# Kernel optimization log

Hardware: AMD Instinct MI355X
Metric: run time of the kernel (lower is better)

The kernel has to match this reference:

```python
import jax, jax.numpy as jnp
import numpy as np

N = 100000   # nodes
E = 3200000  # edges (avg degree 32)
D = 512      # dim_latent
NEG_SLOPE = 0.01  # nn.LeakyReLU default


def setup_inputs() -> dict:
    key = jax.random.key(0)
    ks = jax.random.split(key, 14)
    weight = jax.random.normal(ks[0], (N,), dtype=jnp.float32)
    significance = jax.random.randint(ks[1], (N,), 0, 2, dtype=jnp.int32)
    src = jax.random.randint(ks[2], (E,), 0, N, dtype=jnp.int32)
    dst = jax.random.randint(ks[3], (E,), 0, N, dtype=jnp.int32)
    emb_table = jax.random.normal(ks[4], (2, 2), dtype=jnp.float32)
    lin_W = jax.random.normal(ks[5], (3, D), dtype=jnp.float32) / np.sqrt(3.0)
    lin_b = jnp.zeros((D,), dtype=jnp.float32)
    s = 1.0 / np.sqrt(D)
    W0 = jax.random.normal(ks[6], (D, D), dtype=jnp.float32) * s
    b0 = jnp.zeros((D,), dtype=jnp.float32)
    W1 = jax.random.normal(ks[7], (D, D), dtype=jnp.float32) * s
    b1 = jnp.zeros((D,), dtype=jnp.float32)
    W2 = jax.random.normal(ks[8], (D, D), dtype=jnp.float32) * s
    b2 = jnp.zeros((D,), dtype=jnp.float32)
    pred_W = jax.random.normal(ks[9], (D, 1), dtype=jnp.float32) * s
    pred_b = jnp.zeros((1,), dtype=jnp.float32)
    return {"weight": weight, "significance": significance, "src": src, "dst": dst,
            "emb_table": emb_table, "lin_W": lin_W, "lin_b": lin_b,
            "W0": W0, "b0": b0, "W1": W1, "b1": b1, "W2": W2, "b2": b2,
            "pred_W": pred_W, "pred_b": pred_b}


def _gcn_layer(feat, src, dst, n_out, n_in, W, b):
    # DGL GraphConv norm='both' with self-loops already folded into degrees.
    h = feat * n_out[:, None]                                   # [N, D] src-normalize
    agg = jax.ops.segment_sum(h[src], dst, num_segments=N)      # SpMM aggregate
    agg = agg + h                                               # self-loop message
    agg = agg * n_in[:, None]                                   # dst-normalize
    return agg @ W + b


def reference(weight, significance, src, dst, emb_table, lin_W, lin_b,
              W0, b0, W1, b1, W2, b2, pred_W, pred_b):
    ones = jnp.ones((E,), dtype=jnp.float32)
    deg_out = jax.ops.segment_sum(ones, src, num_segments=N) + 1.0  # +1 self-loop
    deg_in = jax.ops.segment_sum(ones, dst, num_segments=N) + 1.0
    n_out = jax.lax.rsqrt(deg_out)
    n_in = jax.lax.rsqrt(deg_in)

    sig = emb_table[significance]                            # [N, 2]
    feats = jnp.concatenate([weight[:, None], sig], axis=1)  # [N, 3]
    feats = feats @ lin_W + lin_b                            # [N, D]

    h = _gcn_layer(feats, src, dst, n_out, n_in, W0, b0)
    for W, b in ((W1, b1), (W2, b2)):
        h = jnp.where(h >= 0, h, NEG_SLOPE * h)              # LeakyReLU
        h = _gcn_layer(h, src, dst, n_out, n_in, W, b)

    # NOTE: original forward's `if self.train:` is always truthy (method object),
    # so it always returns the prediction logits.
    logits = h @ pred_W + pred_b                             # [N, 1]
    return logits
```

## Files before the change

kernel.cpp:

```cpp
#include <hip/hip_runtime.h>

#define N_NODES 100000
#define M_PAD 100096
#define N_EDGES 3200000
#define DIM 512
#define SLOTS 80
#define NEG_SLOPE 0.01f

typedef _Float16 f16;
typedef _Float16 f16x8 __attribute__((ext_vector_type(8)));
typedef float f32x4 __attribute__((ext_vector_type(4)));

__device__ __forceinline__ void load_lds16(const void* g, void* l) {
  __builtin_amdgcn_global_load_lds(
      (const __attribute__((address_space(1))) void*)g,
      (__attribute__((address_space(3))) void*)l, 16, 0, 0);
}


__global__ void k_pre(const int* __restrict__ src, const int* __restrict__ dst,
                      int* __restrict__ cnt_o, int* __restrict__ cnt_i,
                      int* __restrict__ ell) {
  int e = blockIdx.x * blockDim.x + threadIdx.x;
  if (e < N_EDGES) {
    int s = src[e];
    atomicAdd(&cnt_o[s], 1);
    int d = dst[e];
    int p = atomicAdd(&cnt_i[d], 1);
    if (p < SLOTS) ell[(size_t)d * SLOTS + p] = s;
  }
}

__global__ void k_norms(const int* __restrict__ cnt_o, const int* __restrict__ cnt_i,
                        float* __restrict__ n_out, float* __restrict__ n_in) {
  int i = blockIdx.x * blockDim.x + threadIdx.x;
  if (i < N_NODES) {
    n_out[i] = rsqrtf((float)cnt_o[i] + 1.0f);
    n_in[i] = rsqrtf((float)cnt_i[i] + 1.0f);
  }
}

__global__ void k_wt(const float* __restrict__ W0, const float* __restrict__ W1,
                     f16* __restrict__ Wt) {
  int idx = blockIdx.x * blockDim.x + threadIdx.x;
  int l = idx >> 18;
  int r = idx & 262143;
  int n = r >> 9, k = r & 511;
  const float* W = (l == 0) ? W0 : W1;
  Wt[idx] = (f16)W[k * DIM + n];
}

__global__ void k_wp(const float* __restrict__ W2, const float* __restrict__ b2,
                     const float* __restrict__ pW, const float* __restrict__ pb,
                     float* __restrict__ wt_vec, float* __restrict__ c_out) {
  int k = blockIdx.x, lane = threadIdx.x;
  if (k < DIM) {
    float s = 0.f;
    for (int n = lane; n < DIM; n += 64) s += W2[k * DIM + n] * pW[n];
#pragma unroll
    for (int off = 32; off; off >>= 1) s += __shfl_down(s, off, 64);
    if (lane == 0) wt_vec[k] = s;
  } else {
    float s = 0.f;
    for (int n = lane; n < DIM; n += 64) s += b2[n] * pW[n];
#pragma unroll
    for (int off = 32; off; off >>= 1) s += __shfl_down(s, off, 64);
    if (lane == 0) c_out[0] = s + pb[0];
  }
}


__global__ void k_feats(const float* __restrict__ weight, const int* __restrict__ sig,
                        const float* __restrict__ emb, const float* __restrict__ linW,
                        const float* __restrict__ linb, const float* __restrict__ n_out,
                        f16* __restrict__ Xs) {
  int wid = threadIdx.x >> 6, lane = threadIdx.x & 63;
  int node = blockIdx.x * 4 + wid;
  float w = weight[node];
  int sg = sig[node];
  float s0 = emb[sg * 2], s1 = emb[sg * 2 + 1];
  float no = n_out[node];
  int d0 = lane * 8;
  f16x8 v;
#pragma unroll
  for (int k = 0; k < 8; k++) {
    int d = d0 + k;
    float f = (w * linW[d] + s0 * linW[DIM + d] + s1 * linW[2 * DIM + d] + linb[d]) * no;
    v[k] = (f16)f;
  }
  *(f16x8*)(Xs + (size_t)node * DIM + d0) = v;
}

__global__ void k_spmm(const f16* __restrict__ Xs, f16* __restrict__ A,
                       const int* __restrict__ ell, const int* __restrict__ cnt_i,
                       const float* __restrict__ n_in) {
  int wid = threadIdx.x >> 6, lane = threadIdx.x & 63;
  int node = blockIdx.x * 4 + wid;
  int d0 = lane * 8;
  float acc[8];
  {
    f16x8 v = *(const f16x8*)(Xs + (size_t)node * DIM + d0);
#pragma unroll
    for (int k = 0; k < 8; k++) acc[k] = (float)v[k];
  }
  int deg = cnt_i[node];
  if (deg > SLOTS) deg = SLOTS;
  const int* erow = ell + (size_t)node * SLOTS;
  const f16* base = Xs + d0;
  int j = 0;
  for (; j + 8 <= deg; j += 8) {
    int ix[8];
#pragma unroll
    for (int u = 0; u < 8; u++) ix[u] = erow[j + u];
    f16x8 v[8];
#pragma unroll
    for (int u = 0; u < 8; u++) v[u] = *(const f16x8*)(base + (size_t)ix[u] * DIM);
#pragma unroll
    for (int u = 0; u < 8; u++)
#pragma unroll
      for (int k = 0; k < 8; k++) acc[k] += (float)v[u][k];
  }
  for (; j < deg; ++j) {
    int sn = erow[j];
    f16x8 v = *(const f16x8*)(base + (size_t)sn * DIM);
#pragma unroll
    for (int k = 0; k < 8; k++) acc[k] += (float)v[k];
  }
  float ni = n_in[node];
  f16x8 o;
#pragma unroll
  for (int k = 0; k < 8; k++) o[k] = (f16)(acc[k] * ni);
  __builtin_nontemporal_store(o, (f16x8*)(A + (size_t)node * DIM + d0));
}

__global__ __launch_bounds__(256) void k_gemm(const f16* __restrict__ A, const f16* __restrict__ Wt,
                                              const float* __restrict__ bias,
                                              const float* __restrict__ n_out,
                                              f16* __restrict__ Y,
                                              const float* __restrict__ wt_vec,
                                              float* __restrict__ yv) {
  __shared__ __align__(1024) char smem[32768];
  __shared__ float yred[128];
  const int tid = threadIdx.x;
  const int wid = tid >> 6, lane = tid & 63;
  const int lr = lane & 15, lk = lane >> 4;
  const int wr = wid >> 1, wc = wid & 1;
  const int cb = blockIdx.x * 128;
  const int rb = blockIdx.y * 128;
  const int ls = lane >> 3;
  const int ss = lane & 7;

  f32x4 acc[4][4];
#pragma unroll
  for (int i = 0; i < 4; i++)
#pragma unroll
    for (int j = 0; j < 4; j++) acc[i][j] = (f32x4){0.f, 0.f, 0.f, 0.f};

  for (int kb = 0; kb < DIM; kb += 64) {
#pragma unroll
    for (int i = 0; i < 4; i++) {
      int c = wid * 4 + i;
      int r = c * 8 + ls;
      int goff = (ss * 16) ^ ((r & 7) << 4);
      const char* ga = (const char*)A + ((size_t)(rb + r) * DIM + kb) * 2 + goff;
      load_lds16(ga, smem + c * 1024);
      const char* gw = (const char*)Wt + ((size_t)(cb + r) * DIM + kb) * 2 + goff;
      load_lds16(gw, smem + 16384 + c * 1024);
    }
    __syncthreads();
#pragma unroll
    for (int kk = 0; kk < 2; kk++) {
      f16x8 a[4], b[4];
#pragma unroll
      for (int fm = 0; fm < 4; fm++) {
        int row = wr * 64 + fm * 16 + lr;
        int byt = row * 128 + ((kk * 64 + lk * 16) ^ ((row & 7) << 4));
        a[fm] = *(const f16x8*)(smem + byt);
      }
#pragma unroll
      for (int fn = 0; fn < 4; fn++) {
        int row = wc * 64 + fn * 16 + lr;
        int byt = row * 128 + ((kk * 64 + lk * 16) ^ ((row & 7) << 4));
        b[fn] = *(const f16x8*)(smem + 16384 + byt);
      }
#pragma unroll
      for (int fm = 0; fm < 4; fm++)
#pragma unroll
        for (int fn = 0; fn < 4; fn++)
          acc[fm][fn] = __builtin_amdgcn_mfma_f32_16x16x32_f16(a[fm], b[fn], acc[fm][fn], 0, 0, 0);
    }
    __syncthreads();
  }

  if (yv == nullptr) {
#pragma unroll
    for (int fn = 0; fn < 4; fn++) {
      int col = cb + wc * 64 + fn * 16 + lr;
      float bv = bias[col];
#pragma unroll
      for (int fm = 0; fm < 4; fm++) {
#pragma unroll
        for (int r = 0; r < 4; r++) {
          int row = rb + wr * 64 + fm * 16 + lk * 4 + r;
          if (row < N_NODES) {
            float v = acc[fm][fn][r] + bv;
            v = (v >= 0.f) ? v : NEG_SLOPE * v;
            v *= n_out[row];
            Y[(size_t)row * DIM + col] = (f16)v;
          }
        }
      }
    }
  } else {
    if (tid < 128) yred[tid] = 0.f;
    __syncthreads();
#pragma unroll
    for (int fm = 0; fm < 4; fm++) {
#pragma unroll
      for (int r = 0; r < 4; r++) {
        int rloc = wr * 64 + fm * 16 + lk * 4 + r;
        int row = rb + rloc;
        float p = 0.f;
#pragma unroll
        for (int fn = 0; fn < 4; fn++) {
          int col = cb + wc * 64 + fn * 16 + lr;
          float v = acc[fm][fn][r] + bias[col];
          v = (v >= 0.f) ? v : NEG_SLOPE * v;
          p += v * wt_vec[col];
        }
        if (row < N_NODES) atomicAdd(&yred[rloc], p * n_out[row]);
      }
    }
    __syncthreads();
    if (tid < 128) {
      int row = rb + tid;
      if (row < N_NODES) atomicAdd(&yv[row], yred[tid]);
    }
  }
}

__global__ void k_sagg(const float* __restrict__ y, const int* __restrict__ ell,
                       const int* __restrict__ cnt_i, const float* __restrict__ n_in,
                       const float* __restrict__ c_out, float* __restrict__ out) {
  int i = blockIdx.x * blockDim.x + threadIdx.x;
  if (i >= N_NODES) return;
  int deg = cnt_i[i];
  if (deg > SLOTS) deg = SLOTS;
  const int* erow = ell + (size_t)i * SLOTS;
  float s = y[i];
  int j = 0;
  for (; j + 8 <= deg; j += 8) {
    int4 a = *(const int4*)(erow + j);
    int4 b = *(const int4*)(erow + j + 4);
    s += y[a.x] + y[a.y] + y[a.z] + y[a.w];
    s += y[b.x] + y[b.y] + y[b.z] + y[b.w];
  }
  for (; j < deg; ++j) s += y[erow[j]];
  out[i] = n_in[i] * s + c_out[0];
}

extern "C" void kernel_launch(void* const* d_in, const int* in_sizes, int n_in_cnt,
                              void* d_out, int out_size, void* d_ws, size_t ws_size,
                              hipStream_t stream) {
  const float* weight = (const float*)d_in[0];
  const int* sig = (const int*)d_in[1];
  const int* src = (const int*)d_in[2];
  const int* dst = (const int*)d_in[3];
  const float* emb = (const float*)d_in[4];
  const float* linW = (const float*)d_in[5];
  const float* linb = (const float*)d_in[6];
  const float* W0 = (const float*)d_in[7];
  const float* b0 = (const float*)d_in[8];
  const float* W1 = (const float*)d_in[9];
  const float* b1 = (const float*)d_in[10];
  const float* W2 = (const float*)d_in[11];
  const float* b2 = (const float*)d_in[12];
  const float* pW = (const float*)d_in[13];
  const float* pb = (const float*)d_in[14];
  float* out = (float*)d_out;

  char* ws = (char*)d_ws;
  size_t off = 0;
  auto alloc = [&](size_t bytes) {
    void* p = ws + off;
    off += (bytes + 255) & ~(size_t)255;
    return p;
  };
  int* cnt_o = (int*)alloc((size_t)N_NODES * 4);
  int* cnt_i = (int*)alloc((size_t)N_NODES * 4);
  float* yv = (float*)alloc((size_t)N_NODES * 4);
  float* n_out = (float*)alloc((size_t)N_NODES * 4);
  float* n_in = (float*)alloc((size_t)N_NODES * 4);
  int* ell = (int*)alloc((size_t)N_NODES * SLOTS * 4);
  f16* Wt = (f16*)alloc((size_t)2 * DIM * DIM * 2);
  float* wt_vec = (float*)alloc((size_t)DIM * 4);
  float* c_out = (float*)alloc(256);
  f16* B0 = (f16*)alloc((size_t)M_PAD * DIM * 2);
  f16* B1 = (f16*)alloc((size_t)M_PAD * DIM * 2);

  dim3 blk(256);
  hipMemsetAsync(cnt_o, 0, (char*)n_out - (char*)cnt_o, stream);
  k_pre<<<(N_EDGES + 255) / 256, blk, 0, stream>>>(src, dst, cnt_o, cnt_i, ell);
  k_norms<<<(N_NODES + 255) / 256, blk, 0, stream>>>(cnt_o, cnt_i, n_out, n_in);
  k_wt<<<2 * DIM * DIM / 256, blk, 0, stream>>>(W0, W1, Wt);
  k_wp<<<DIM + 1, 64, 0, stream>>>(W2, b2, pW, pb, wt_vec, c_out);
  k_feats<<<N_NODES / 4, blk, 0, stream>>>(weight, sig, emb, linW, linb, n_out, B0);

  dim3 ggrid(DIM / 128, M_PAD / 128);
  k_spmm<<<N_NODES / 4, blk, 0, stream>>>(B0, B1, ell, cnt_i, n_in);
  k_gemm<<<ggrid, blk, 0, stream>>>(B1, Wt, b0, n_out, B0, nullptr, nullptr);
  k_spmm<<<N_NODES / 4, blk, 0, stream>>>(B0, B1, ell, cnt_i, n_in);
  k_gemm<<<ggrid, blk, 0, stream>>>(B1, Wt + (size_t)DIM * DIM, b1, n_out, nullptr, wt_vec, yv);
  k_sagg<<<(N_NODES + 255) / 256, blk, 0, stream>>>(yv, ell, cnt_i, n_in, c_out, out);
}
```

Before: 1.651 ms.

## Merge setup kernels into one launch and move source normalization into SpMM

Four setup kernels (edge counting/ELL build, weight transpose, predictor fold, input features) become one kernel whose block index ranges select the work, so they can overlap and launch overhead drops. The feature kernel no longer depends on n_out, which is what allows the merge. Source-degree scaling moves out of feature creation and the GEMM epilogue and into the SpMM gather, which now loads n_out per neighbor. This adds a scalar gather per edge in each SpMM pass and keeps unnormalized values in fp16, which slightly changes rounding.

```diff
diff --git a/kernel.cpp b/kernel.cpp
--- a/kernel.cpp
+++ b/kernel.cpp
@@ -7,6 +7,11 @@
 #define SLOTS 80
 #define NEG_SLOPE 0.01f
 
+#define B_PRE 12500
+#define B_WT (B_PRE + 2048)
+#define B_WP (B_WT + 129)
+#define B_FEAT (B_WP + 25000)
+
 typedef _Float16 f16;
 typedef _Float16 f16x8 __attribute__((ext_vector_type(8)));
 typedef float f32x4 __attribute__((ext_vector_type(4)));
@@ -17,17 +22,65 @@
       (__attribute__((address_space(3))) void*)l, 16, 0, 0);
 }
 
-
-__global__ void k_pre(const int* __restrict__ src, const int* __restrict__ dst,
-                      int* __restrict__ cnt_o, int* __restrict__ cnt_i,
-                      int* __restrict__ ell) {
-  int e = blockIdx.x * blockDim.x + threadIdx.x;
-  if (e < N_EDGES) {
+__global__ void k_setup(const int* __restrict__ src, const int* __restrict__ dst,
+                        int* __restrict__ cnt_o, int* __restrict__ cnt_i,
+                        int* __restrict__ ell,
+                        const float* __restrict__ W0, const float* __restrict__ W1,
+                        f16* __restrict__ Wt,
+                        const float* __restrict__ W2, const float* __restrict__ b2,
+                        const float* __restrict__ pW, const float* __restrict__ pb,
+                        float* __restrict__ wt_vec, float* __restrict__ c_out,
+                        const float* __restrict__ weight, const int* __restrict__ sig,
+                        const float* __restrict__ emb, const float* __restrict__ linW,
+                        const float* __restrict__ linb, f16* __restrict__ Xs) {
+  const int bid = blockIdx.x;
+  const int tid = threadIdx.x;
+  if (bid < B_PRE) {
+    int e = bid * 256 + tid;
     int s = src[e];
     atomicAdd(&cnt_o[s], 1);
     int d = dst[e];
     int p = atomicAdd(&cnt_i[d], 1);
     if (p < SLOTS) ell[(size_t)d * SLOTS + p] = s;
+  } else if (bid < B_WT) {
+    int idx = (bid - B_PRE) * 256 + tid;
+    int l = idx >> 18;
+    int r = idx & 262143;
+    int n = r >> 9, k = r & 511;
+    const float* W = l ? W1 : W0;
+    Wt[idx] = (f16)W[k * DIM + n];
+  } else if (bid < B_WP) {
+    int wid = tid >> 6, lane = tid & 63;
+    int t = (bid - B_WT) * 4 + wid;
+    if (t < DIM) {
+      float s = 0.f;
+#pragma unroll
+      for (int n = 0; n < DIM; n += 64) s += W2[t * DIM + n + lane] * pW[n + lane];
+#pragma unroll
+      for (int off = 32; off; off >>= 1) s += __shfl_down(s, off, 64);
+      if (lane == 0) wt_vec[t] = s;
+    } else if (t == DIM) {
+      float s = 0.f;
+#pragma unroll
+      for (int n = 0; n < DIM; n += 64) s += b2[n + lane] * pW[n + lane];
+#pragma unroll
+      for (int off = 32; off; off >>= 1) s += __shfl_down(s, off, 64);
+      if (lane == 0) c_out[0] = s + pb[0];
+    }
+  } else {
+    int wid = tid >> 6, lane = tid & 63;
+    int node = (bid - B_WP) * 4 + wid;
+    float w = weight[node];
+    int sg = sig[node];
+    float s0 = emb[sg * 2], s1 = emb[sg * 2 + 1];
+    int d0 = lane * 8;
+    f16x8 v;
+#pragma unroll
+    for (int k = 0; k < 8; k++) {
+      int d = d0 + k;
+      v[k] = (f16)(w * linW[d] + s0 * linW[DIM + d] + s1 * linW[2 * DIM + d] + linb[d]);
+    }
+    *(f16x8*)(Xs + (size_t)node * DIM + d0) = v;
   }
 }
 
@@ -40,68 +93,19 @@
   }
 }
 
-__global__ void k_wt(const float* __restrict__ W0, const float* __restrict__ W1,
-                     f16* __restrict__ Wt) {
-  int idx = blockIdx.x * blockDim.x + threadIdx.x;
-  int l = idx >> 18;
-  int r = idx & 262143;
-  int n = r >> 9, k = r & 511;
-  const float* W = (l == 0) ? W0 : W1;
-  Wt[idx] = (f16)W[k * DIM + n];
-}
-
-__global__ void k_wp(const float* __restrict__ W2, const float* __restrict__ b2,
-                     const float* __restrict__ pW, const float* __restrict__ pb,
-                     float* __restrict__ wt_vec, float* __restrict__ c_out) {
-  int k = blockIdx.x, lane = threadIdx.x;
-  if (k < DIM) {
-    float s = 0.f;
-    for (int n = lane; n < DIM; n += 64) s += W2[k * DIM + n] * pW[n];
-#pragma unroll
-    for (int off = 32; off; off >>= 1) s += __shfl_down(s, off, 64);
-    if (lane == 0) wt_vec[k] = s;
-  } else {
-    float s = 0.f;
-    for (int n = lane; n < DIM; n += 64) s += b2[n] * pW[n];
-#pragma unroll
-    for (int off = 32; off; off >>= 1) s += __shfl_down(s, off, 64);
-    if (lane == 0) c_out[0] = s + pb[0];
-  }
-}
-
-
-__global__ void k_feats(const float* __restrict__ weight, const int* __restrict__ sig,
-                        const float* __restrict__ emb, const float* __restrict__ linW,
-                        const float* __restrict__ linb, const float* __restrict__ n_out,
-                        f16* __restrict__ Xs) {
-  int wid = threadIdx.x >> 6, lane = threadIdx.x & 63;
-  int node = blockIdx.x * 4 + wid;
-  float w = weight[node];
-  int sg = sig[node];
-  float s0 = emb[sg * 2], s1 = emb[sg * 2 + 1];
-  float no = n_out[node];
-  int d0 = lane * 8;
-  f16x8 v;
-#pragma unroll
-  for (int k = 0; k < 8; k++) {
-    int d = d0 + k;
-    float f = (w * linW[d] + s0 * linW[DIM + d] + s1 * linW[2 * DIM + d] + linb[d]) * no;
-    v[k] = (f16)f;
-  }
-  *(f16x8*)(Xs + (size_t)node * DIM + d0) = v;
-}
 
 __global__ void k_spmm(const f16* __restrict__ Xs, f16* __restrict__ A,
                        const int* __restrict__ ell, const int* __restrict__ cnt_i,
-                       const float* __restrict__ n_in) {
+                       const float* __restrict__ n_in, const float* __restrict__ n_out) {
   int wid = threadIdx.x >> 6, lane = threadIdx.x & 63;
   int node = blockIdx.x * 4 + wid;
   int d0 = lane * 8;
   float acc[8];
   {
     f16x8 v = *(const f16x8*)(Xs + (size_t)node * DIM + d0);
-#pragma unroll
-    for (int k = 0; k < 8; k++) acc[k] = (float)v[k];
+    float no = n_out[node];
+#pragma unroll
+    for (int k = 0; k < 8; k++) acc[k] = no * (float)v[k];
   }
   int deg = cnt_i[node];
   if (deg > SLOTS) deg = SLOTS;
@@ -112,19 +116,23 @@
     int ix[8];
 #pragma unroll
     for (int u = 0; u < 8; u++) ix[u] = erow[j + u];
+    float sc[8];
+#pragma unroll
+    for (int u = 0; u < 8; u++) sc[u] = n_out[ix[u]];
     f16x8 v[8];
 #pragma unroll
     for (int u = 0; u < 8; u++) v[u] = *(const f16x8*)(base + (size_t)ix[u] * DIM);
 #pragma unroll
     for (int u = 0; u < 8; u++)
 #pragma unroll
-      for (int k = 0; k < 8; k++) acc[k] += (float)v[u][k];
+      for (int k = 0; k < 8; k++) acc[k] += sc[u] * (float)v[u][k];
   }
   for (; j < deg; ++j) {
     int sn = erow[j];
+    float sc = n_out[sn];
     f16x8 v = *(const f16x8*)(base + (size_t)sn * DIM);
 #pragma unroll
-    for (int k = 0; k < 8; k++) acc[k] += (float)v[k];
+    for (int k = 0; k < 8; k++) acc[k] += sc * (float)v[k];
   }
   float ni = n_in[node];
   f16x8 o;
@@ -205,7 +213,6 @@
           if (row < N_NODES) {
             float v = acc[fm][fn][r] + bv;
             v = (v >= 0.f) ? v : NEG_SLOPE * v;
-            v *= n_out[row];
             Y[(size_t)row * DIM + col] = (f16)v;
           }
         }
@@ -300,16 +307,15 @@
 
   dim3 blk(256);
   hipMemsetAsync(cnt_o, 0, (char*)n_out - (char*)cnt_o, stream);
-  k_pre<<<(N_EDGES + 255) / 256, blk, 0, stream>>>(src, dst, cnt_o, cnt_i, ell);
+  k_setup<<<B_FEAT, blk, 0, stream>>>(src, dst, cnt_o, cnt_i, ell,
+                                      W0, W1, Wt, W2, b2, pW, pb, wt_vec, c_out,
+                                      weight, sig, emb, linW, linb, B0);
   k_norms<<<(N_NODES + 255) / 256, blk, 0, stream>>>(cnt_o, cnt_i, n_out, n_in);
-  k_wt<<<2 * DIM * DIM / 256, blk, 0, stream>>>(W0, W1, Wt);
-  k_wp<<<DIM + 1, 64, 0, stream>>>(W2, b2, pW, pb, wt_vec, c_out);
-  k_feats<<<N_NODES / 4, blk, 0, stream>>>(weight, sig, emb, linW, linb, n_out, B0);
 
   dim3 ggrid(DIM / 128, M_PAD / 128);
-  k_spmm<<<N_NODES / 4, blk, 0, stream>>>(B0, B1, ell, cnt_i, n_in);
+  k_spmm<<<N_NODES / 4, blk, 0, stream>>>(B0, B1, ell, cnt_i, n_in, n_out);
   k_gemm<<<ggrid, blk, 0, stream>>>(B1, Wt, b0, n_out, B0, nullptr, nullptr);
-  k_spmm<<<N_NODES / 4, blk, 0, stream>>>(B0, B1, ell, cnt_i, n_in);
+  k_spmm<<<N_NODES / 4, blk, 0, stream>>>(B0, B1, ell, cnt_i, n_in, n_out);
   k_gemm<<<ggrid, blk, 0, stream>>>(B1, Wt + (size_t)DIM * DIM, b1, n_out, nullptr, wt_vec, yv);
   k_sagg<<<(N_NODES + 255) / 256, blk, 0, stream>>>(yv, ell, cnt_i, n_in, c_out, out);
 }
```

Measured after the change: 1.640 ms. No clear change (-0.7%).
